# Kernel tuning notes

Measured on AMD Instinct MI355X. Metric: run time of the kernel, lower is better.

The kernel has to match this reference:

```python
import jax, jax.numpy as jnp
import numpy as np

MARGIN = 1.0
NUM_CLASSES = 1024


def setup_inputs() -> dict:
    key = jax.random.key(0)
    k1, k2 = jax.random.split(key)
    embeddings = jax.random.normal(k1, (8192, 128), dtype=jnp.float32)
    labels = jax.random.randint(k2, (8192,), 0, NUM_CLASSES, dtype=jnp.int64)
    return {"embeddings": embeddings, "labels": labels}


def reference(embeddings, labels):
    """Triplet loss with hard-negative mining, fully vectorized.

    Matches TripletLossWithMining(margin=1.0, mining_strategy='hard'):
      - squared-Euclidean pairwise distance matrix, relu-clamped, zero diagonal
      - for every (anchor i, positive p): hardest negative n* = argmin_{n: label!=label_i} d[i,n]
      - triplet kept iff d[i,n*] < d[i,p]; loss = mean relu(d[i,p] - d[i,n*] + margin)
    """
    B = embeddings.shape[0]
    sq = jnp.sum(embeddings * embeddings, axis=1, keepdims=True)          # [B,1]
    dist = sq + sq.T - 2.0 * (embeddings @ embeddings.T)                   # [B,B]
    dist = jax.nn.relu(dist)
    eye = jnp.eye(B, dtype=bool)
    dist = jnp.where(eye, jnp.zeros((), dist.dtype), dist)                 # fill_diagonal_(0)

    same = labels[:, None] == labels[None, :]                              # [B,B]
    pos_mask = same & ~eye
    neg_mask = ~same
    has_neg = jnp.any(neg_mask, axis=1)                                    # [B]

    # hardest (closest) negative per anchor
    neg_d = jnp.where(neg_mask, dist, jnp.array(jnp.inf, dist.dtype))
    hardest_neg = jnp.min(neg_d, axis=1)                                   # [B]

    # triplet (i,p) is kept iff p is a valid positive, i has a negative,
    # and hardest_neg[i] < pos_dist d[i,p]
    valid = pos_mask & has_neg[:, None] & (hardest_neg[:, None] < dist)    # [B,B]

    per_triplet = jax.nn.relu(dist - hardest_neg[:, None] + MARGIN)        # [B,B]
    count = jnp.sum(valid)
    total = jnp.sum(jnp.where(valid, per_triplet, jnp.zeros((), dist.dtype)))
    loss = total / jnp.maximum(count, 1).astype(dist.dtype)
    return loss, count
```

## Files before the change

kernel.cpp:

```cpp
#include <hip/hip_runtime.h>
#include <stdint.h>

#define BB 8192
#define DD 128
#define MARGIN 1.0f
#define CCAP 48
#define NBLK_POS (BB / 4)
#define NCH 16
#define CHCOLS (BB / NCH)
#define TPC (CHCOLS / 64)

typedef __attribute__((ext_vector_type(8))) short short8_t;
typedef __attribute__((ext_vector_type(4))) float f32x4;

#define GLL16(g, l)                                                                   \
  __builtin_amdgcn_global_load_lds(                                                   \
      (const __attribute__((address_space(1))) unsigned int*)(g),                     \
      (__attribute__((address_space(3))) unsigned int*)(l), 16, 0, 0)

__device__ __forceinline__ unsigned short f2bf(float f) {
  unsigned u = __float_as_uint(f);
  u = (u + 0x7fffu + ((u >> 16) & 1u)) >> 16;
  return (unsigned short)u;
}

__global__ void prep_kernel(const float* __restrict__ E, const int* __restrict__ lab,
                            unsigned short* __restrict__ Ebf,
                            float* __restrict__ sq,
                            int* __restrict__ cls_cnt, int* __restrict__ cls_idx) {
  int wid = threadIdx.x >> 6, lane = threadIdx.x & 63;
  int row = blockIdx.x * 4 + wid;
  const float2 v = *(const float2*)(E + (size_t)row * DD + lane * 2);
  ushort2 bb;
  bb.x = f2bf(v.x);
  bb.y = f2bf(v.y);
  *(ushort2*)(Ebf + (size_t)row * DD + lane * 2) = bb;
  float s = v.x * v.x + v.y * v.y;
  for (int off = 1; off < 64; off <<= 1) s += __shfl_xor(s, off);
  if (lane == 0) {
    sq[row] = s;
    int labi = lab[row];
    int p = atomicAdd(&cls_cnt[labi], 1);
    if (p < CCAP) cls_idx[labi * CCAP + p] = row;
  }
}

__global__ __launch_bounds__(256) void dist_min_kernel(
    const unsigned short* __restrict__ Ebf, const float* __restrict__ sq,
    const int* __restrict__ lab, float* __restrict__ part) {
  __shared__ __align__(16) char ldsA[128 * 256];
  __shared__ __align__(16) char ldsB[2][64 * 256];
  __shared__ int labC[CHCOLS];
  __shared__ float hC[CHCOLS];
  __shared__ int labI[128];
  __shared__ float redMin[4][64];

  const int tid = threadIdx.x;
  const int p = blockIdx.x >> 4, c = blockIdx.x & (NCH - 1);
  const int rI = p * 128;
  const int cBase = c * CHCOLS;

  const int wid = tid >> 6, lane = tid & 63;
  const int l4 = lane >> 4, c16 = lane & 15;
  const int wr = wid >> 1, wc = wid & 1;
  const int rowbase = wr * 64;
  const int cl = c16, rg = l4;

#define STAGE_A()                                                                   \
  {                                                                                 \
    _Pragma("unroll") for (int q = 0; q < 8; q++) {                                 \
      int r = wid * 32 + q * 4 + l4;                                                \
      int chunk = c16 ^ (r & 7);                                                    \
      GLL16((const char*)Ebf + (size_t)(rI + r) * 256 + chunk * 16,                 \
            ldsA + wid * 8192 + q * 1024);                                          \
    }                                                                               \
  }
#define STAGE_B(tt, buf)                                                            \
  {                                                                                 \
    _Pragma("unroll") for (int q = 0; q < 4; q++) {                                 \
      int r = wid * 16 + q * 4 + l4;                                                \
      int chunk = c16 ^ (r & 7);                                                    \
      GLL16((const char*)Ebf + (size_t)(cBase + (tt)*64 + r) * 256 + chunk * 16,    \
            (buf) + wid * 4096 + q * 1024);                                         \
    }                                                                               \
  }

  STAGE_A();
  STAGE_B(0, ldsB[0]);
  STAGE_B(1, ldsB[1]);

  for (int q = tid; q < CHCOLS; q += 256) {
    labC[q] = lab[cBase + q];
    hC[q] = 0.5f * sq[cBase + q];
  }
  if (tid < 128) labI[tid] = lab[rI + tid];

  int il[4][4];
  float tm[4][4];
#pragma unroll
  for (int m = 0; m < 4; m++)
#pragma unroll
    for (int r = 0; r < 4; r++) tm[m][r] = __builtin_huge_valf();

#pragma unroll
  for (int t = 0; t < TPC; t++) {
    if (t < TPC - 1)
      asm volatile("s_waitcnt vmcnt(4) lgkmcnt(0)" ::: "memory");
    else
      asm volatile("s_waitcnt vmcnt(0) lgkmcnt(0)" ::: "memory");
    __builtin_amdgcn_sched_barrier(0);
    __builtin_amdgcn_s_barrier();
    __builtin_amdgcn_sched_barrier(0);

    if (t == 0) {
#pragma unroll
      for (int m = 0; m < 4; m++)
#pragma unroll
        for (int r = 0; r < 4; r++) il[m][r] = labI[rowbase + m * 16 + rg * 4 + r];
    }

    int jl[2];
    float jh[2];
#pragma unroll
    for (int n = 0; n < 2; n++) {
      int j = t * 64 + wc * 32 + n * 16 + cl;
      jl[n] = labC[j];
      jh[n] = hC[j];
    }

    f32x4 acc[4][2];
#pragma unroll
    for (int m = 0; m < 4; m++)
#pragma unroll
      for (int n = 0; n < 2; n++) acc[m][n] = (f32x4){0.f, 0.f, 0.f, 0.f};

#pragma unroll
    for (int kk = 0; kk < 4; kk++) {
      const int kb = kk * 64 + rg * 16;
      short8_t a[4], b[2];
#pragma unroll
      for (int m = 0; m < 4; m++) {
        int row = rowbase + m * 16 + cl;
        a[m] = *(const short8_t*)(ldsA + row * 256 + (kb ^ ((row & 7) << 4)));
      }
#pragma unroll
      for (int n = 0; n < 2; n++) {
        int row = wc * 32 + n * 16 + cl;
        b[n] = *(const short8_t*)(ldsB[t & 1] + row * 256 + (kb ^ ((row & 7) << 4)));
      }
#pragma unroll
      for (int m = 0; m < 4; m++)
#pragma unroll
        for (int n = 0; n < 2; n++)
          acc[m][n] = __builtin_amdgcn_mfma_f32_16x16x32_bf16(a[m], b[n], acc[m][n], 0, 0, 0);
    }

#pragma unroll
    for (int m = 0; m < 4; m++)
#pragma unroll
      for (int n = 0; n < 2; n++) {
        f32x4 v = acc[m][n];
#pragma unroll
        for (int r = 0; r < 4; r++) {
          float u = jh[n] - v[r];
          if (il[m][r] != jl[n]) tm[m][r] = fminf(tm[m][r], u);
        }
      }

    __builtin_amdgcn_s_barrier();
    __builtin_amdgcn_sched_barrier(0);
    if (t + 2 < TPC) STAGE_B(t + 2, ldsB[t & 1]);
  }

#pragma unroll
  for (int m = 0; m < 4; m++)
#pragma unroll
    for (int r = 0; r < 4; r++) {
      float t = tm[m][r];
      t = fminf(t, __shfl_xor(t, 1));
      t = fminf(t, __shfl_xor(t, 2));
      t = fminf(t, __shfl_xor(t, 4));
      t = fminf(t, __shfl_xor(t, 8));
      tm[m][r] = t;
    }
  if (cl == 0) {
#pragma unroll
    for (int m = 0; m < 4; m++)
#pragma unroll
      for (int r = 0; r < 4; r++) redMin[wid][m * 16 + rg * 4 + r] = tm[m][r];
  }
  __syncthreads();
  if (wc == 0) {
    float v = fminf(redMin[wid][lane], redMin[wid + 1][lane]);
    part[(size_t)c * BB + rI + rowbase + lane] = v;
  }
}

__global__ void pos_loss_kernel(const float* __restrict__ E, const int* __restrict__ lab,
                                const float* __restrict__ sq, const float* __restrict__ part,
                                const int* __restrict__ cls_cnt, const int* __restrict__ cls_idx,
                                float* __restrict__ ptot, int* __restrict__ pcnt) {
  __shared__ float stot[4];
  __shared__ int scnt[4];
  const int tid = threadIdx.x, wid = tid >> 6, lane = tid & 63;
  const int i = blockIdx.x * 4 + wid;
  const int labi = lab[i];
  int n = cls_cnt[labi];
  if (n > CCAP) n = CCAP;
  const float2 ei = *(const float2*)(E + (size_t)i * DD + lane * 2);
  const float sqi = sq[i];
  float mn = __builtin_huge_valf();
#pragma unroll
  for (int cc = 0; cc < NCH; cc++) mn = fminf(mn, part[(size_t)cc * BB + i]);
  const float hn = fmaxf(sqi + 2.0f * mn, 0.0f);
  float tsum = 0.0f;
  int tcnt = 0;
  for (int s = 0; s < n; s++) {
    int j = cls_idx[labi * CCAP + s];
    if (j == i) continue;
    float2 ej = *(const float2*)(E + (size_t)j * DD + lane * 2);
    float pp = ei.x * ej.x + ei.y * ej.y;
    for (int off = 1; off < 64; off <<= 1) pp += __shfl_xor(pp, off);
    float d = fmaxf(sqi + sq[j] - 2.0f * pp, 0.0f);
    if (hn < d) {
      tcnt++;
      tsum += d - hn + MARGIN;
    }
  }
  if (lane == 0) {
    stot[wid] = tsum;
    scnt[wid] = tcnt;
  }
  __syncthreads();
  if (tid == 0) {
    ptot[blockIdx.x] = stot[0] + stot[1] + stot[2] + stot[3];
    pcnt[blockIdx.x] = scnt[0] + scnt[1] + scnt[2] + scnt[3];
  }
}

__global__ void finalize_kernel(const float* __restrict__ ptot, const int* __restrict__ pcnt,
                                float* __restrict__ out) {
  __shared__ float stot[4];
  __shared__ int scnt[4];
  const int tid = threadIdx.x, wid = tid >> 6, lane = tid & 63;
  float t = 0.0f;
  int c = 0;
  for (int k = tid; k < NBLK_POS; k += 256) {
    t += ptot[k];
    c += pcnt[k];
  }
  for (int off = 1; off < 64; off <<= 1) {
    t += __shfl_xor(t, off);
    c += __shfl_xor(c, off);
  }
  if (lane == 0) {
    stot[wid] = t;
    scnt[wid] = c;
  }
  __syncthreads();
  if (tid == 0) {
    float tt = stot[0] + stot[1] + stot[2] + stot[3];
    int cc = scnt[0] + scnt[1] + scnt[2] + scnt[3];
    out[0] = tt / (float)(cc > 0 ? cc : 1);
    out[1] = (float)cc;
  }
}

extern "C" void kernel_launch(void* const* d_in, const int* in_sizes, int n_in,
                              void* d_out, int out_size, void* d_ws, size_t ws_size,
                              hipStream_t stream) {
  const float* E = (const float*)d_in[0];
  const int* lab = (const int*)d_in[1];
  float* out = (float*)d_out;

  char* ws = (char*)d_ws;
  unsigned short* Ebf = (unsigned short*)ws;
  float* sq = (float*)(ws + (size_t)BB * DD * 2);
  int* cls_cnt = (int*)((char*)sq + BB * 4);
  int* cls_idx = (int*)((char*)cls_cnt + 1024 * 4);
  float* ptot = (float*)((char*)cls_idx + 1024 * CCAP * 4);
  int* pcnt = (int*)((char*)ptot + NBLK_POS * 4);
  float* part = (float*)((char*)pcnt + NBLK_POS * 4);

  hipMemsetAsync(cls_cnt, 0, 1024 * 4, stream);
  prep_kernel<<<BB / 4, 256, 0, stream>>>(E, lab, Ebf, sq, cls_cnt, cls_idx);
  dist_min_kernel<<<64 * NCH, 256, 0, stream>>>(Ebf, sq, lab, part);
  pos_loss_kernel<<<NBLK_POS, 256, 0, stream>>>(E, lab, sq, part, cls_cnt, cls_idx, ptot, pcnt);
  finalize_kernel<<<1, 256, 0, stream>>>(ptot, pcnt, out);
}
```

Measured before the change: 112.7 us.

## Fuse all stages into one persistent kernel with atomic grid barriers

```diff
diff --git a/kernel.cpp b/kernel.cpp
--- a/kernel.cpp
+++ b/kernel.cpp
@@ -5,10 +5,11 @@
 #define DD 128
 #define MARGIN 1.0f
 #define CCAP 48
-#define NBLK_POS (BB / 4)
-#define NCH 16
+#define NCH 8
 #define CHCOLS (BB / NCH)
 #define TPC (CHCOLS / 64)
+#define NBLK 512
+#define RPB 16
 
 typedef __attribute__((ext_vector_type(8))) short short8_t;
 typedef __attribute__((ext_vector_type(4))) float f32x4;
@@ -24,30 +25,23 @@
   return (unsigned short)u;
 }
 
-__global__ void prep_kernel(const float* __restrict__ E, const int* __restrict__ lab,
-                            unsigned short* __restrict__ Ebf,
-                            float* __restrict__ sq,
-                            int* __restrict__ cls_cnt, int* __restrict__ cls_idx) {
-  int wid = threadIdx.x >> 6, lane = threadIdx.x & 63;
-  int row = blockIdx.x * 4 + wid;
-  const float2 v = *(const float2*)(E + (size_t)row * DD + lane * 2);
-  ushort2 bb;
-  bb.x = f2bf(v.x);
-  bb.y = f2bf(v.y);
-  *(ushort2*)(Ebf + (size_t)row * DD + lane * 2) = bb;
-  float s = v.x * v.x + v.y * v.y;
-  for (int off = 1; off < 64; off <<= 1) s += __shfl_xor(s, off);
-  if (lane == 0) {
-    sq[row] = s;
-    int labi = lab[row];
-    int p = atomicAdd(&cls_cnt[labi], 1);
-    if (p < CCAP) cls_idx[labi * CCAP + p] = row;
-  }
+__device__ __forceinline__ void gridbar(unsigned* c) {
+  __syncthreads();
+  if (threadIdx.x == 0) {
+    __threadfence();
+    atomicAdd(c, 1u);
+    while (atomicAdd(c, 0u) < NBLK) __builtin_amdgcn_s_sleep(32);
+    __threadfence();
+  }
+  __syncthreads();
 }
 
-__global__ __launch_bounds__(256) void dist_min_kernel(
-    const unsigned short* __restrict__ Ebf, const float* __restrict__ sq,
-    const int* __restrict__ lab, float* __restrict__ part) {
+__global__ __launch_bounds__(256, 2) void fused_kernel(
+    const float* __restrict__ E, const int* __restrict__ lab,
+    unsigned short* __restrict__ Ebf, float* __restrict__ sq,
+    int* __restrict__ cls_cnt, int* __restrict__ cls_idx,
+    float* __restrict__ part, float* __restrict__ ptot, int* __restrict__ pcnt,
+    unsigned* __restrict__ ctr, float* __restrict__ out) {
   __shared__ __align__(16) char ldsA[128 * 256];
   __shared__ __align__(16) char ldsB[2][64 * 256];
   __shared__ int labC[CHCOLS];
@@ -56,15 +50,36 @@
   __shared__ float redMin[4][64];
 
   const int tid = threadIdx.x;
-  const int p = blockIdx.x >> 4, c = blockIdx.x & (NCH - 1);
-  const int rI = p * 128;
-  const int cBase = c * CHCOLS;
-
+  const int b = blockIdx.x;
   const int wid = tid >> 6, lane = tid & 63;
   const int l4 = lane >> 4, c16 = lane & 15;
-  const int wr = wid >> 1, wc = wid & 1;
-  const int rowbase = wr * 64;
-  const int cl = c16, rg = l4;
+
+#pragma unroll
+  for (int rr = 0; rr < 4; rr++) {
+    int row = b * RPB + wid * 4 + rr;
+    const float2 v = *(const float2*)(E + (size_t)row * DD + lane * 2);
+    ushort2 bb;
+    bb.x = f2bf(v.x);
+    bb.y = f2bf(v.y);
+    *(ushort2*)(Ebf + (size_t)row * DD + lane * 2) = bb;
+    float s = v.x * v.x + v.y * v.y;
+    for (int off = 1; off < 64; off <<= 1) s += __shfl_xor(s, off);
+    if (lane == 0) {
+      sq[row] = s;
+      int labi = lab[row];
+      int pp = atomicAdd(&cls_cnt[labi], 1);
+      if (pp < CCAP) cls_idx[labi * CCAP + pp] = row;
+    }
+  }
+  gridbar(&ctr[0]);
+
+  {
+    const int p = b >> 3, c = b & (NCH - 1);
+    const int rI = p * 128;
+    const int cBase = c * CHCOLS;
+    const int wr = wid >> 1, wc = wid & 1;
+    const int rowbase = wr * 64;
+    const int cl = c16, rg = l4;
 
 #define STAGE_A()                                                                   \
   {                                                                                 \
@@ -85,184 +100,183 @@
     }                                                                               \
   }
 
-  STAGE_A();
-  STAGE_B(0, ldsB[0]);
-  STAGE_B(1, ldsB[1]);
-
-  for (int q = tid; q < CHCOLS; q += 256) {
-    labC[q] = lab[cBase + q];
-    hC[q] = 0.5f * sq[cBase + q];
-  }
-  if (tid < 128) labI[tid] = lab[rI + tid];
-
-  int il[4][4];
-  float tm[4][4];
-#pragma unroll
-  for (int m = 0; m < 4; m++)
-#pragma unroll
-    for (int r = 0; r < 4; r++) tm[m][r] = __builtin_huge_valf();
-
-#pragma unroll
-  for (int t = 0; t < TPC; t++) {
-    if (t < TPC - 1)
-      asm volatile("s_waitcnt vmcnt(4) lgkmcnt(0)" ::: "memory");
-    else
-      asm volatile("s_waitcnt vmcnt(0) lgkmcnt(0)" ::: "memory");
-    __builtin_amdgcn_sched_barrier(0);
-    __builtin_amdgcn_s_barrier();
-    __builtin_amdgcn_sched_barrier(0);
-
-    if (t == 0) {
+    STAGE_A();
+    STAGE_B(0, ldsB[0]);
+    STAGE_B(1, ldsB[1]);
+
+    for (int q = tid; q < CHCOLS; q += 256) {
+      labC[q] = lab[cBase + q];
+      hC[q] = 0.5f * sq[cBase + q];
+    }
+    if (tid < 128) labI[tid] = lab[rI + tid];
+
+    int il[4][4];
+    float tm[4][4];
+#pragma unroll
+    for (int m = 0; m < 4; m++)
+#pragma unroll
+      for (int r = 0; r < 4; r++) tm[m][r] = __builtin_huge_valf();
+
+#pragma unroll 2
+    for (int t = 0; t < TPC; t++) {
+      if (t < TPC - 1)
+        asm volatile("s_waitcnt vmcnt(4) lgkmcnt(0)" ::: "memory");
+      else
+        asm volatile("s_waitcnt vmcnt(0) lgkmcnt(0)" ::: "memory");
+      __builtin_amdgcn_sched_barrier(0);
+      __builtin_amdgcn_s_barrier();
+      __builtin_amdgcn_sched_barrier(0);
+
+      if (t == 0) {
+#pragma unroll
+        for (int m = 0; m < 4; m++)
+#pragma unroll
+          for (int r = 0; r < 4; r++) il[m][r] = labI[rowbase + m * 16 + rg * 4 + r];
+      }
+
+      int jl[2];
+      float jh[2];
+#pragma unroll
+      for (int n = 0; n < 2; n++) {
+        int j = t * 64 + wc * 32 + n * 16 + cl;
+        jl[n] = labC[j];
+        jh[n] = hC[j];
+      }
+
+      f32x4 acc[4][2];
 #pragma unroll
       for (int m = 0; m < 4; m++)
 #pragma unroll
-        for (int r = 0; r < 4; r++) il[m][r] = labI[rowbase + m * 16 + rg * 4 + r];
-    }
-
-    int jl[2];
-    float jh[2];
-#pragma unroll
-    for (int n = 0; n < 2; n++) {
-      int j = t * 64 + wc * 32 + n * 16 + cl;
-      jl[n] = labC[j];
-      jh[n] = hC[j];
-    }
-
-    f32x4 acc[4][2];
+        for (int n = 0; n < 2; n++) acc[m][n] = (f32x4){0.f, 0.f, 0.f, 0.f};
+
+#pragma unroll
+      for (int kk = 0; kk < 4; kk++) {
+        const int kb = kk * 64 + rg * 16;
+        short8_t a[4], bfr[2];
+#pragma unroll
+        for (int m = 0; m < 4; m++) {
+          int row = rowbase + m * 16 + cl;
+          a[m] = *(const short8_t*)(ldsA + row * 256 + (kb ^ ((row & 7) << 4)));
+        }
+#pragma unroll
+        for (int n = 0; n < 2; n++) {
+          int row = wc * 32 + n * 16 + cl;
+          bfr[n] = *(const short8_t*)(ldsB[t & 1] + row * 256 + (kb ^ ((row & 7) << 4)));
+        }
+#pragma unroll
+        for (int m = 0; m < 4; m++)
+#pragma unroll
+          for (int n = 0; n < 2; n++)
+            acc[m][n] = __builtin_amdgcn_mfma_f32_16x16x32_bf16(a[m], bfr[n], acc[m][n], 0, 0, 0);
+      }
+
+#pragma unroll
+      for (int m = 0; m < 4; m++)
+#pragma unroll
+        for (int n = 0; n < 2; n++) {
+          f32x4 v = acc[m][n];
+#pragma unroll
+          for (int r = 0; r < 4; r++) {
+            float u = jh[n] - v[r];
+            if (il[m][r] != jl[n]) tm[m][r] = fminf(tm[m][r], u);
+          }
+        }
+
+      __builtin_amdgcn_s_barrier();
+      __builtin_amdgcn_sched_barrier(0);
+      if (t + 2 < TPC) STAGE_B(t + 2, ldsB[t & 1]);
+    }
+
 #pragma unroll
     for (int m = 0; m < 4; m++)
 #pragma unroll
-      for (int n = 0; n < 2; n++) acc[m][n] = (f32x4){0.f, 0.f, 0.f, 0.f};
-
-#pragma unroll
-    for (int kk = 0; kk < 4; kk++) {
-      const int kb = kk * 64 + rg * 16;
-      short8_t a[4], b[2];
-#pragma unroll
-      for (int m = 0; m < 4; m++) {
-        int row = rowbase + m * 16 + cl;
-        a[m] = *(const short8_t*)(ldsA + row * 256 + (kb ^ ((row & 7) << 4)));
-      }
-#pragma unroll
-      for (int n = 0; n < 2; n++) {
-        int row = wc * 32 + n * 16 + cl;
-        b[n] = *(const short8_t*)(ldsB[t & 1] + row * 256 + (kb ^ ((row & 7) << 4)));
-      }
+      for (int r = 0; r < 4; r++) {
+        float t = tm[m][r];
+        t = fminf(t, __shfl_xor(t, 1));
+        t = fminf(t, __shfl_xor(t, 2));
+        t = fminf(t, __shfl_xor(t, 4));
+        t = fminf(t, __shfl_xor(t, 8));
+        tm[m][r] = t;
+      }
+    if (cl == 0) {
 #pragma unroll
       for (int m = 0; m < 4; m++)
 #pragma unroll
-        for (int n = 0; n < 2; n++)
-          acc[m][n] = __builtin_amdgcn_mfma_f32_16x16x32_bf16(a[m], b[n], acc[m][n], 0, 0, 0);
-    }
-
-#pragma unroll
-    for (int m = 0; m < 4; m++)
-#pragma unroll
-      for (int n = 0; n < 2; n++) {
-        f32x4 v = acc[m][n];
-#pragma unroll
-        for (int r = 0; r < 4; r++) {
-          float u = jh[n] - v[r];
-          if (il[m][r] != jl[n]) tm[m][r] = fminf(tm[m][r], u);
+        for (int r = 0; r < 4; r++) redMin[wid][m * 16 + rg * 4 + r] = tm[m][r];
+    }
+    __syncthreads();
+    if (wc == 0) {
+      float v = fminf(redMin[wid][lane], redMin[wid + 1][lane]);
+      part[(size_t)c * BB + rI + rowbase + lane] = v;
+    }
+  }
+  gridbar(&ctr[1]);
+
+  {
+    float tsum = 0.0f;
+    int tcnt = 0;
+#pragma unroll
+    for (int aa = 0; aa < 4; aa++) {
+      const int i = b * RPB + wid * 4 + aa;
+      const int labi = lab[i];
+      int n = cls_cnt[labi];
+      if (n > CCAP) n = CCAP;
+      const float2 ei = *(const float2*)(E + (size_t)i * DD + lane * 2);
+      const float sqi = sq[i];
+      float mn = __builtin_huge_valf();
+#pragma unroll
+      for (int cc = 0; cc < NCH; cc++) mn = fminf(mn, part[(size_t)cc * BB + i]);
+      const float hn = fmaxf(sqi + 2.0f * mn, 0.0f);
+      for (int s = 0; s < n; s++) {
+        int j = cls_idx[labi * CCAP + s];
+        if (j == i) continue;
+        float2 ej = *(const float2*)(E + (size_t)j * DD + lane * 2);
+        float pp = ei.x * ej.x + ei.y * ej.y;
+        for (int off = 1; off < 64; off <<= 1) pp += __shfl_xor(pp, off);
+        float d = fmaxf(sqi + sq[j] - 2.0f * pp, 0.0f);
+        if (hn < d) {
+          tcnt++;
+          tsum += d - hn + MARGIN;
         }
       }
-
-    __builtin_amdgcn_s_barrier();
-    __builtin_amdgcn_sched_barrier(0);
-    if (t + 2 < TPC) STAGE_B(t + 2, ldsB[t & 1]);
-  }
-
-#pragma unroll
-  for (int m = 0; m < 4; m++)
-#pragma unroll
-    for (int r = 0; r < 4; r++) {
-      float t = tm[m][r];
-      t = fminf(t, __shfl_xor(t, 1));
-      t = fminf(t, __shfl_xor(t, 2));
-      t = fminf(t, __shfl_xor(t, 4));
-      t = fminf(t, __shfl_xor(t, 8));
-      tm[m][r] = t;
-    }
-  if (cl == 0) {
-#pragma unroll
-    for (int m = 0; m < 4; m++)
-#pragma unroll
-      for (int r = 0; r < 4; r++) redMin[wid][m * 16 + rg * 4 + r] = tm[m][r];
-  }
-  __syncthreads();
-  if (wc == 0) {
-    float v = fminf(redMin[wid][lane], redMin[wid + 1][lane]);
-    part[(size_t)c * BB + rI + rowbase + lane] = v;
-  }
-}
-
-__global__ void pos_loss_kernel(const float* __restrict__ E, const int* __restrict__ lab,
-                                const float* __restrict__ sq, const float* __restrict__ part,
-                                const int* __restrict__ cls_cnt, const int* __restrict__ cls_idx,
-                                float* __restrict__ ptot, int* __restrict__ pcnt) {
-  __shared__ float stot[4];
-  __shared__ int scnt[4];
-  const int tid = threadIdx.x, wid = tid >> 6, lane = tid & 63;
-  const int i = blockIdx.x * 4 + wid;
-  const int labi = lab[i];
-  int n = cls_cnt[labi];
-  if (n > CCAP) n = CCAP;
-  const float2 ei = *(const float2*)(E + (size_t)i * DD + lane * 2);
-  const float sqi = sq[i];
-  float mn = __builtin_huge_valf();
-#pragma unroll
-  for (int cc = 0; cc < NCH; cc++) mn = fminf(mn, part[(size_t)cc * BB + i]);
-  const float hn = fmaxf(sqi + 2.0f * mn, 0.0f);
-  float tsum = 0.0f;
-  int tcnt = 0;
-  for (int s = 0; s < n; s++) {
-    int j = cls_idx[labi * CCAP + s];
-    if (j == i) continue;
-    float2 ej = *(const float2*)(E + (size_t)j * DD + lane * 2);
-    float pp = ei.x * ej.x + ei.y * ej.y;
-    for (int off = 1; off < 64; off <<= 1) pp += __shfl_xor(pp, off);
-    float d = fmaxf(sqi + sq[j] - 2.0f * pp, 0.0f);
-    if (hn < d) {
-      tcnt++;
-      tsum += d - hn + MARGIN;
-    }
-  }
-  if (lane == 0) {
-    stot[wid] = tsum;
-    scnt[wid] = tcnt;
-  }
-  __syncthreads();
-  if (tid == 0) {
-    ptot[blockIdx.x] = stot[0] + stot[1] + stot[2] + stot[3];
-    pcnt[blockIdx.x] = scnt[0] + scnt[1] + scnt[2] + scnt[3];
-  }
-}
-
-__global__ void finalize_kernel(const float* __restrict__ ptot, const int* __restrict__ pcnt,
-                                float* __restrict__ out) {
-  __shared__ float stot[4];
-  __shared__ int scnt[4];
-  const int tid = threadIdx.x, wid = tid >> 6, lane = tid & 63;
-  float t = 0.0f;
-  int c = 0;
-  for (int k = tid; k < NBLK_POS; k += 256) {
-    t += ptot[k];
-    c += pcnt[k];
-  }
-  for (int off = 1; off < 64; off <<= 1) {
-    t += __shfl_xor(t, off);
-    c += __shfl_xor(c, off);
-  }
-  if (lane == 0) {
-    stot[wid] = t;
-    scnt[wid] = c;
-  }
-  __syncthreads();
-  if (tid == 0) {
-    float tt = stot[0] + stot[1] + stot[2] + stot[3];
-    int cc = scnt[0] + scnt[1] + scnt[2] + scnt[3];
-    out[0] = tt / (float)(cc > 0 ? cc : 1);
-    out[1] = (float)cc;
+    }
+    if (lane == 0) {
+      redMin[0][wid] = tsum;
+      ((int*)&redMin[1][0])[wid] = tcnt;
+    }
+    __syncthreads();
+    if (tid == 0) {
+      ptot[b] = redMin[0][0] + redMin[0][1] + redMin[0][2] + redMin[0][3];
+      int* sc = (int*)&redMin[1][0];
+      pcnt[b] = sc[0] + sc[1] + sc[2] + sc[3];
+    }
+  }
+  gridbar(&ctr[2]);
+
+  if (b == 0) {
+    float t = 0.0f;
+    int c = 0;
+    for (int k = tid; k < NBLK; k += 256) {
+      t += ptot[k];
+      c += pcnt[k];
+    }
+    for (int off = 1; off < 64; off <<= 1) {
+      t += __shfl_xor(t, off);
+      c += __shfl_xor(c, off);
+    }
+    __syncthreads();
+    if (lane == 0) {
+      redMin[2][wid] = t;
+      ((int*)&redMin[3][0])[wid] = c;
+    }
+    __syncthreads();
+    if (tid == 0) {
+      float tt = redMin[2][0] + redMin[2][1] + redMin[2][2] + redMin[2][3];
+      int* sc = (int*)&redMin[3][0];
+      int cc = sc[0] + sc[1] + sc[2] + sc[3];
+      out[0] = tt / (float)(cc > 0 ? cc : 1);
+      out[1] = (float)cc;
+    }
   }
 }
 
@@ -275,16 +289,15 @@
 
   char* ws = (char*)d_ws;
   unsigned short* Ebf = (unsigned short*)ws;
-  float* sq = (float*)(ws + (size_t)BB * DD * 2);
-  int* cls_cnt = (int*)((char*)sq + BB * 4);
-  int* cls_idx = (int*)((char*)cls_cnt + 1024 * 4);
-  float* ptot = (float*)((char*)cls_idx + 1024 * CCAP * 4);
-  int* pcnt = (int*)((char*)ptot + NBLK_POS * 4);
-  float* part = (float*)((char*)pcnt + NBLK_POS * 4);
-
-  hipMemsetAsync(cls_cnt, 0, 1024 * 4, stream);
-  prep_kernel<<<BB / 4, 256, 0, stream>>>(E, lab, Ebf, sq, cls_cnt, cls_idx);
-  dist_min_kernel<<<64 * NCH, 256, 0, stream>>>(Ebf, sq, lab, part);
-  pos_loss_kernel<<<NBLK_POS, 256, 0, stream>>>(E, lab, sq, part, cls_cnt, cls_idx, ptot, pcnt);
-  finalize_kernel<<<1, 256, 0, stream>>>(ptot, pcnt, out);
+  float* sq = (float*)(ws + 2097152);
+  int* cls_cnt = (int*)(ws + 2129920);
+  unsigned* ctr = (unsigned*)(ws + 2134016);
+  int* cls_idx = (int*)(ws + 2134080);
+  float* part = (float*)(ws + 2330688);
+  float* ptot = (float*)(ws + 2592832);
+  int* pcnt = (int*)(ws + 2594880);
+
+  hipMemsetAsync(cls_cnt, 0, 4096 + 64, stream);
+  fused_kernel<<<NBLK, 256, 0, stream>>>(E, lab, Ebf, sq, cls_cnt, cls_idx,
+                                         part, ptot, pcnt, ctr, out);
 }
```

Result: slower. 251.7 us (+123.4%).
